# Kernel tuning notes

Hardware: AMD Instinct MI355X
Metric: run time of the kernel (lower is better)

## Reference

```python
import jax, jax.numpy as jnp
import numpy as np

N = 262144   # active voxels
C = 128      # channels (in == out)
B, Z, Y, X = 2, 41, 512, 512
EPS = 1e-3   # BN eps from norm_cfg


def _build_neighbors():
    """Build submanifold rulebook-style neighbor tables along z, y, x axes.
    Each table is [N, 3] (offsets -1, 0, +1); missing neighbor -> sentinel N
    (points at a zero-padded feature row)."""
    rng = np.random.default_rng(0)
    total = B * Z * Y * X
    lin = np.sort(rng.choice(total, size=N, replace=False)).astype(np.int64)
    lookup = np.full(total, -1, dtype=np.int64)
    lookup[lin] = np.arange(N)
    r = lin % (Z * Y * X)
    z = r // (Y * X)
    r2 = r % (Y * X)
    y = r2 // X
    x = r2 % X

    def nbrs(axis_vals, axis_size, stride):
        cols = []
        for off in (-1, 0, 1):
            v = axis_vals + off
            valid = (v >= 0) & (v < axis_size)
            nlin = np.clip(lin + off * stride, 0, total - 1)
            idx = np.where(valid, lookup[nlin], -1)
            idx = np.where(idx < 0, N, idx)
            cols.append(idx)
        return np.stack(cols, axis=1).astype(np.int32)

    return nbrs(z, Z, Y * X), nbrs(y, Y, X), nbrs(x, X, 1)


def setup_inputs() -> dict:
    key = jax.random.key(0)
    ks = jax.random.split(key, 8)
    nbr_z, nbr_y, nbr_x = _build_neighbors()
    scale = 1.0 / np.sqrt(3 * C)
    inp = {
        "features": jax.random.normal(ks[0], (N, C), dtype=jnp.float32),
        "W1": jax.random.normal(ks[1], (3, C, C), dtype=jnp.float32) * scale,  # conv3x1x1
        "W2": jax.random.normal(ks[2], (3, C, C), dtype=jnp.float32) * scale,  # conv1x3x1
        "W3": jax.random.normal(ks[3], (3, C, C), dtype=jnp.float32) * scale,  # conv1x1x3
        "g0": jax.random.normal(ks[4], (C,), dtype=jnp.float32) * 0.1 + 1.0,
        "b0": jnp.zeros((C,), dtype=jnp.float32),
        "m0": jax.random.normal(ks[5], (C,), dtype=jnp.float32) * 0.1,
        "v0": jax.random.uniform(ks[5], (C,), minval=0.5, maxval=1.5, dtype=jnp.float32),
        "g2": jax.random.normal(ks[6], (C,), dtype=jnp.float32) * 0.1 + 1.0,
        "b2": jnp.zeros((C,), dtype=jnp.float32),
        "m2": jax.random.normal(ks[6], (C,), dtype=jnp.float32) * 0.1,
        "v2": jax.random.uniform(ks[6], (C,), minval=0.5, maxval=1.5, dtype=jnp.float32),
        "g3": jax.random.normal(ks[7], (C,), dtype=jnp.float32) * 0.1 + 1.0,
        "b3": jnp.zeros((C,), dtype=jnp.float32),
        "m3": jax.random.normal(ks[7], (C,), dtype=jnp.float32) * 0.1,
        "v3": jax.random.uniform(ks[7], (C,), minval=0.5, maxval=1.5, dtype=jnp.float32),
        "nbr_z": jnp.asarray(nbr_z),
        "nbr_y": jnp.asarray(nbr_y),
        "nbr_x": jnp.asarray(nbr_x),
    }
    return inp


def _subm_conv(feats, nbr, W):
    # submanifold gather-matmul: out[n] = sum_k W[k] @ feats[nbr[n,k]] (sentinel -> 0)
    feats_pad = jnp.concatenate([feats, jnp.zeros((1, feats.shape[1]), feats.dtype)], axis=0)
    gathered = feats_pad[nbr]  # [N, 3, C]
    return jnp.einsum('nkc,kcd->nd', gathered, W)


def _bn(x, g, b, m, v):
    return (x - m) * (g * jax.lax.rsqrt(v + EPS)) + b


def reference(features, W1, W2, W3, g0, b0, m0, v0, g2, b2, m2, v2,
              g3, b3, m3, v3, nbr_z, nbr_y, nbr_x):
    # Branch 1: conv3x1x1 -> bn0 -> sigmoid, then (source bug) bn0_2 -> sigmoid applied again
    s = jax.nn.sigmoid(_bn(_subm_conv(features, nbr_z, W1), g0, b0, m0, v0))
    s = jax.nn.sigmoid(_bn(s, g2, b2, m2, v2))
    # Branch 2: conv1x3x1, added raw (its BN/act were mistakenly applied to branch 1)
    s2 = _subm_conv(features, nbr_y, W2)
    # Branch 3: conv1x1x3 -> bn0_3 -> sigmoid
    s3 = jax.nn.sigmoid(_bn(_subm_conv(features, nbr_x, W3), g3, b3, m3, v3))
    return (s + s2 + s3) * features
```

## Files before the change

### kernel.cpp

```cpp
#include <hip/hip_runtime.h>
#include <hip/hip_bf16.h>
#include <stdint.h>
#include <stddef.h>

#define NVOX 262144
#define CCH 128
#define BN_EPS 1e-3f

typedef __attribute__((ext_vector_type(8))) short bfrag;
typedef __attribute__((ext_vector_type(4))) float f4;

#define AS1 __attribute__((address_space(1)))
#define AS3 __attribute__((address_space(3)))

__device__ __forceinline__ unsigned short f2bf(float f) {
  union { float f; unsigned u; } v; v.f = f;
  unsigned r = v.u + 0x7fffu + ((v.u >> 16) & 1u);
  return (unsigned short)(r >> 16);
}

__device__ __forceinline__ bfrag pack8(f4 x, f4 y) {
  bfrag r;
  r[0] = (short)f2bf(x[0]); r[1] = (short)f2bf(x[1]);
  r[2] = (short)f2bf(x[2]); r[3] = (short)f2bf(x[3]);
  r[4] = (short)f2bf(y[0]); r[5] = (short)f2bf(y[1]);
  r[6] = (short)f2bf(y[2]); r[7] = (short)f2bf(y[3]);
  return r;
}

__device__ __forceinline__ float sigmoidf_(float x) {
  return 1.f / (1.f + __expf(-x));
}

__device__ __forceinline__ float bf2f(unsigned short h) {
  union { unsigned u; float f; } v; v.u = ((unsigned)h) << 16; return v.f;
}

__global__ void prep_wfrag(const float* __restrict__ W1, const float* __restrict__ W2,
                           const float* __restrict__ W3, unsigned short* __restrict__ wf) {
  const int frag = blockIdx.x;
  const int tile = frag & 7;
  const int kc   = (frag >> 3) & 3;
  const int tap  = (frag >> 5) % 3;
  const int conv = frag / 96;
  const float* W = (conv == 0) ? W1 : ((conv == 1) ? W2 : W3);
  const int l   = threadIdx.x;
  const int col = tile * 16 + (l & 15);
  const int k0  = kc * 32 + (l >> 4) * 8;
  bfrag o;
#pragma unroll
  for (int e = 0; e < 8; ++e)
    o[e] = (short)f2bf(W[(size_t)(tap * CCH + k0 + e) * CCH + col]);
  *reinterpret_cast<bfrag*>(wf + (size_t)frag * 512 + l * 8) = o;
}

__global__ void prep_bn(const float* g0, const float* b0, const float* m0, const float* v0,
                        const float* g2, const float* b2, const float* m2, const float* v2,
                        const float* g3, const float* b3, const float* m3, const float* v3,
                        float* __restrict__ bn) {
  const int c = threadIdx.x;
  const float s0 = g0[c] * rsqrtf(v0[c] + BN_EPS);
  const float s2 = g2[c] * rsqrtf(v2[c] + BN_EPS);
  const float s3 = g3[c] * rsqrtf(v3[c] + BN_EPS);
  bn[0 * CCH + c] = s0; bn[1 * CCH + c] = b0[c] - m0[c] * s0;
  bn[2 * CCH + c] = s2; bn[3 * CCH + c] = b2[c] - m2[c] * s2;
  bn[4 * CCH + c] = s3; bn[5 * CCH + c] = b3[c] - m3[c] * s3;
}

__global__ void prep_bf16(const float* __restrict__ feats, unsigned short* __restrict__ fbf) {
  const size_t base = ((size_t)blockIdx.x * 256 + threadIdx.x) * 8;
  const f4 x = *reinterpret_cast<const f4*>(feats + base);
  const f4 y = *reinterpret_cast<const f4*>(feats + base + 4);
  *reinterpret_cast<bfrag*>(fbf + base) = pack8(x, y);
  if (blockIdx.x == 0 && threadIdx.x < 16) {
    bfrag z = {0, 0, 0, 0, 0, 0, 0, 0};
    *reinterpret_cast<bfrag*>(fbf + (size_t)NVOX * CCH + threadIdx.x * 8) = z;
  }
}

__global__ __launch_bounds__(512, 4)
void recon_v11(const unsigned short* __restrict__ fbf,
               const unsigned short* __restrict__ wfrag,
               const float* __restrict__ bn,
               const int* __restrict__ nbrz, const int* __restrict__ nbrx,
               const int* __restrict__ nbry,
               float* __restrict__ out) {
  __shared__ unsigned short Bb[24576];

  const int tid  = threadIdx.x;
  const int lane = tid & 63;
  const int w    = tid >> 6;
  const int l15  = lane & 15;
  const int lhi  = lane >> 4;
  const int cb   = blockIdx.x & 1;
  const int row0 = (blockIdx.x >> 1) * 128;
  const int wrow = row0 + w * 16;

  auto fillconv = [&](int RB) {
#pragma unroll
    for (int i = 0; i < 6; ++i) {
      const int L    = w * 6 + i;
      const int slot = L >> 4;
      const int sub  = L & 15;
      const int g    = ((RB + slot) * 4 + (sub >> 2)) * 8 + cb * 4 + (sub & 3);
      __builtin_amdgcn_global_load_lds(
          (const AS1 void*)(wfrag + (size_t)g * 512 + lane * 8),
          (AS3 void*)((char*)Bb + L * 1024), 16, 0, 0);
    }
  };

  fillconv(0);
  const int row = wrow + l15;
  const int rg  = row * 3;
  const int izp = nbrz[rg + 0], izn = nbrz[rg + 2];
  const int ixp = nbrx[rg + 0], ixn = nbrx[rg + 2];
  const int iyp = nbry[rg + 0], iyn = nbry[rg + 2];

  const bool azp = __any(izp != NVOX), azn = __any(izn != NVOX);
  const bool axp = __any(ixp != NVOX), axn = __any(ixn != NVOX);
  const bool ayp = __any(iyp != NVOX), ayn = __any(iyn != NVOX);

  bfrag aF[4];
  bfrag aS[4];

#define LOADF(DST, IDX) {                                                     \
    const char* p = (const char*)fbf + ((size_t)(unsigned)(IDX) << 8) + (lhi << 4); \
    DST[0] = *reinterpret_cast<const bfrag*>(p);                              \
    DST[1] = *reinterpret_cast<const bfrag*>(p + 64);                         \
    DST[2] = *reinterpret_cast<const bfrag*>(p + 128);                        \
    DST[3] = *reinterpret_cast<const bfrag*>(p + 192);                        \
  }

#define TAP(SLOT, AFR, ACCS) {                                                \
    const char* bs = (const char*)Bb + (SLOT) * 16384 + lane * 16;            \
    _Pragma("unroll")                                                         \
    for (int kc = 0; kc < 4; ++kc) {                                          \
      _Pragma("unroll")                                                       \
      for (int ct = 0; ct < 4; ++ct) {                                        \
        const bfrag b = *reinterpret_cast<const bfrag*>(                      \
            bs + (kc * 4 + ct) * 1024);                                       \
        ACCS[ct] = __builtin_amdgcn_mfma_f32_16x16x32_bf16(                   \
            AFR[kc], b, ACCS[ct], 0, 0, 0);                                   \
      } } }

#define CONV(VP, VN, IP, IN, ACCS)                                            \
  {                                                                           \
    if (VP)      LOADF(aF, IP)                                                \
    else if (VN) LOADF(aF, IN)                                                \
    TAP(1, aS, ACCS)                                                          \
    if (VP) {                                                                 \
      TAP(0, aF, ACCS)                                                        \
      if (VN) { LOADF(aF, IN)  TAP(2, aF, ACCS) }                             \
    } else if (VN) {                                                          \
      TAP(2, aF, ACCS)                                                        \
    }                                                                         \
  }

  LOADF(aS, row)

  __syncthreads();

  f4 acc[4], run[4];
#pragma unroll
  for (int ct = 0; ct < 4; ++ct) {
    acc[ct] = f4{0.f, 0.f, 0.f, 0.f};
    run[ct] = f4{0.f, 0.f, 0.f, 0.f};
  }

  CONV(azp, azn, izp, izn, acc)
  __syncthreads();
  fillconv(6);
#pragma unroll
  for (int ct = 0; ct < 4; ++ct) {
    const int col = cb * 64 + ct * 16 + l15;
    const float sc0 = bn[0 * CCH + col], sh0 = bn[1 * CCH + col];
    const float sc2 = bn[2 * CCH + col], sh2 = bn[3 * CCH + col];
#pragma unroll
    for (int j = 0; j < 4; ++j) {
      const float u = sigmoidf_(sc0 * acc[ct][j] + sh0);
      run[ct][j] = sigmoidf_(sc2 * u + sh2);
    }
    acc[ct] = f4{0.f, 0.f, 0.f, 0.f};
  }
  __syncthreads();

  CONV(axp, axn, ixp, ixn, acc)
  __syncthreads();
  fillconv(3);
#pragma unroll
  for (int ct = 0; ct < 4; ++ct) {
    const int col = cb * 64 + ct * 16 + l15;
    const float sc3 = bn[4 * CCH + col], sh3 = bn[5 * CCH + col];
#pragma unroll
    for (int j = 0; j < 4; ++j)
      run[ct][j] += sigmoidf_(sc3 * acc[ct][j] + sh3);
  }
  __syncthreads();

  CONV(ayp, ayn, iyp, iyn, run)

#undef CONV
#undef TAP
#undef LOADF

#pragma unroll
  for (int ct = 0; ct < 4; ++ct) {
    const int col = cb * 64 + ct * 16 + l15;
#pragma unroll
    for (int j = 0; j < 4; ++j) {
      const int r = wrow + (lhi << 2) + j;
      const size_t o = ((size_t)r << 7) + col;
      out[o] = run[ct][j] * bf2f(fbf[o]);
    }
  }
}

__global__ void recon_naive(const float* __restrict__ feats,
    const float* __restrict__ W1, const float* __restrict__ W2, const float* __restrict__ W3,
    const int* __restrict__ nbrz, const int* __restrict__ nbry, const int* __restrict__ nbrx,
    const float* g0, const float* b0, const float* m0, const float* v0,
    const float* g2, const float* b2, const float* m2, const float* v2,
    const float* g3, const float* b3, const float* m3, const float* v3,
    float* __restrict__ out) {
  __shared__ float rows[3][CCH];
  const int n = blockIdx.x;
  const int d = threadIdx.x;
  float res[3];
#pragma unroll
  for (int conv = 0; conv < 3; ++conv) {
    const int* nbr  = (conv == 0) ? nbrz : ((conv == 1) ? nbry : nbrx);
    const float* W  = (conv == 0) ? W1 : ((conv == 1) ? W2 : W3);
#pragma unroll
    for (int tap = 0; tap < 3; ++tap) {
      const int idx = nbr[n * 3 + tap];
      rows[tap][d] = ((unsigned)idx < (unsigned)NVOX) ? feats[((size_t)idx << 7) + d] : 0.f;
    }
    __syncthreads();
    const float* rflat = &rows[0][0];
    float s = 0.f;
    for (int k = 0; k < 3 * CCH; ++k) s += rflat[k] * W[(size_t)k * CCH + d];
    res[conv] = s;
    __syncthreads();
  }
  const float sc0 = g0[d] * rsqrtf(v0[d] + BN_EPS), sh0 = b0[d] - m0[d] * sc0;
  const float sc2 = g2[d] * rsqrtf(v2[d] + BN_EPS), sh2 = b2[d] - m2[d] * sc2;
  const float sc3 = g3[d] * rsqrtf(v3[d] + BN_EPS), sh3 = b3[d] - m3[d] * sc3;
  float u = sigmoidf_(sc0 * res[0] + sh0);
  u = sigmoidf_(sc2 * u + sh2);
  const float s3v = sigmoidf_(sc3 * res[2] + sh3);
  out[((size_t)n << 7) + d] = (u + res[1] + s3v) * feats[((size_t)n << 7) + d];
}

extern "C" void kernel_launch(void* const* d_in, const int* in_sizes, int n_in,
                              void* d_out, int out_size, void* d_ws, size_t ws_size,
                              hipStream_t stream) {
  const float* feats = (const float*)d_in[0];
  const float* W1 = (const float*)d_in[1];
  const float* W2 = (const float*)d_in[2];
  const float* W3 = (const float*)d_in[3];
  const float* g0 = (const float*)d_in[4];
  const float* b0 = (const float*)d_in[5];
  const float* m0 = (const float*)d_in[6];
  const float* v0 = (const float*)d_in[7];
  const float* g2 = (const float*)d_in[8];
  const float* b2 = (const float*)d_in[9];
  const float* m2 = (const float*)d_in[10];
  const float* v2 = (const float*)d_in[11];
  const float* g3 = (const float*)d_in[12];
  const float* b3 = (const float*)d_in[13];
  const float* m3 = (const float*)d_in[14];
  const float* v3 = (const float*)d_in[15];
  const int* nz = (const int*)d_in[16];
  const int* ny = (const int*)d_in[17];
  const int* nx = (const int*)d_in[18];
  float* out = (float*)d_out;

  const size_t wf_bytes = 288u * 1024u;
  const size_t bn_bytes = 4096u;
  const size_t fb_bytes = ((size_t)NVOX + 1) * CCH * sizeof(short);
  if (ws_size >= wf_bytes + bn_bytes + fb_bytes) {
    unsigned short* wf  = (unsigned short*)d_ws;
    float*          bnt = (float*)((char*)d_ws + wf_bytes);
    unsigned short* fbf = (unsigned short*)((char*)d_ws + wf_bytes + bn_bytes);
    hipLaunchKernelGGL(prep_wfrag, dim3(288), dim3(64), 0, stream, W1, W2, W3, wf);
    hipLaunchKernelGGL(prep_bn, dim3(1), dim3(CCH), 0, stream,
                       g0, b0, m0, v0, g2, b2, m2, v2, g3, b3, m3, v3, bnt);
    hipLaunchKernelGGL(prep_bf16, dim3((NVOX * CCH) / (256 * 8)), dim3(256), 0, stream,
                       feats, fbf);
    hipLaunchKernelGGL(recon_v11, dim3((NVOX / 128) * 2), dim3(512), 0, stream,
                       fbf, wf, bnt, nz, nx, ny, out);
  } else {
    hipLaunchKernelGGL(recon_naive, dim3(NVOX), dim3(CCH), 0, stream,
                       feats, W1, W2, W3, nz, ny, nx,
                       g0, b0, m0, v0, g2, b2, m2, v2, g3, b3, m3, v3, out);
  }
}
```

Before: 149.8 us.

## Process two 16-row tiles per wave to reuse LDS weight fragments

Each wave now computes 32 rows instead of 16, issuing two MFMAs per weight fragment read from LDS. This halves LDS weight traffic and the weight fill per output row, and halves the grid size. A block-index swizzle spreads the 8 blocks of each group across distant row ranges. The centre-tap feature load is no longer kept in registers across convs: it is reloaded per conv, and the tap-skip branches are simplified. Register pressure doubles for the accumulators, which may hurt occupancy under launch_bounds(512,4).

```diff
diff --git a/kernel.cpp b/kernel.cpp
--- a/kernel.cpp
+++ b/kernel.cpp
@@ -79,7 +79,7 @@
 }
 
 __global__ __launch_bounds__(512, 4)
-void recon_v11(const unsigned short* __restrict__ fbf,
+void recon_v12(const unsigned short* __restrict__ fbf,
                const unsigned short* __restrict__ wfrag,
                const float* __restrict__ bn,
                const int* __restrict__ nbrz, const int* __restrict__ nbrx,
@@ -92,9 +92,10 @@
   const int w    = tid >> 6;
   const int l15  = lane & 15;
   const int lhi  = lane >> 4;
-  const int cb   = blockIdx.x & 1;
-  const int row0 = (blockIdx.x >> 1) * 128;
-  const int wrow = row0 + w * 16;
+  const int bid  = ((blockIdx.x & 7) << 8) + (blockIdx.x >> 3);
+  const int cb   = bid & 1;
+  const int row0 = (bid >> 1) << 8;
+  const int wrow = row0 + w * 32;
 
   auto fillconv = [&](int RB) {
 #pragma unroll
@@ -110,18 +111,24 @@
   };
 
   fillconv(0);
-  const int row = wrow + l15;
-  const int rg  = row * 3;
-  const int izp = nbrz[rg + 0], izn = nbrz[rg + 2];
-  const int ixp = nbrx[rg + 0], ixn = nbrx[rg + 2];
-  const int iyp = nbry[rg + 0], iyn = nbry[rg + 2];
-
-  const bool azp = __any(izp != NVOX), azn = __any(izn != NVOX);
-  const bool axp = __any(ixp != NVOX), axn = __any(ixn != NVOX);
-  const bool ayp = __any(iyp != NVOX), ayn = __any(iyn != NVOX);
-
-  bfrag aF[4];
-  bfrag aS[4];
+  const int rowA = wrow + l15;
+  const int rowB = rowA + 16;
+  const int rgA = rowA * 3, rgB = rowB * 3;
+  const int izpA = nbrz[rgA + 0], iznA = nbrz[rgA + 2];
+  const int izpB = nbrz[rgB + 0], iznB = nbrz[rgB + 2];
+  const int ixpA = nbrx[rgA + 0], ixnA = nbrx[rgA + 2];
+  const int ixpB = nbrx[rgB + 0], ixnB = nbrx[rgB + 2];
+  const int iypA = nbry[rgA + 0], iynA = nbry[rgA + 2];
+  const int iypB = nbry[rgB + 0], iynB = nbry[rgB + 2];
+
+  const bool azp = __any((izpA != NVOX) || (izpB != NVOX));
+  const bool azn = __any((iznA != NVOX) || (iznB != NVOX));
+  const bool axp = __any((ixpA != NVOX) || (ixpB != NVOX));
+  const bool axn = __any((ixnA != NVOX) || (ixnB != NVOX));
+  const bool ayp = __any((iypA != NVOX) || (iypB != NVOX));
+  const bool ayn = __any((iynA != NVOX) || (iynB != NVOX));
+
+  bfrag aX[4], aY[4];
 
 #define LOADF(DST, IDX) {                                                     \
     const char* p = (const char*)fbf + ((size_t)(unsigned)(IDX) << 8) + (lhi << 4); \
@@ -131,7 +138,7 @@
     DST[3] = *reinterpret_cast<const bfrag*>(p + 192);                        \
   }
 
-#define TAP(SLOT, AFR, ACCS) {                                                \
+#define TAP2(SLOT, A0, A1) {                                                  \
     const char* bs = (const char*)Bb + (SLOT) * 16384 + lane * 16;            \
     _Pragma("unroll")                                                         \
     for (int kc = 0; kc < 4; ++kc) {                                          \
@@ -139,35 +146,27 @@
       for (int ct = 0; ct < 4; ++ct) {                                        \
         const bfrag b = *reinterpret_cast<const bfrag*>(                      \
             bs + (kc * 4 + ct) * 1024);                                       \
-        ACCS[ct] = __builtin_amdgcn_mfma_f32_16x16x32_bf16(                   \
-            AFR[kc], b, ACCS[ct], 0, 0, 0);                                   \
+        A0[ct] = __builtin_amdgcn_mfma_f32_16x16x32_bf16(aX[kc], b, A0[ct], 0, 0, 0); \
+        A1[ct] = __builtin_amdgcn_mfma_f32_16x16x32_bf16(aY[kc], b, A1[ct], 0, 0, 0); \
       } } }
 
-#define CONV(VP, VN, IP, IN, ACCS)                                            \
+#define CONV(VP, VN, IPA, IPB, INA, INB, A0, A1)                              \
   {                                                                           \
-    if (VP)      LOADF(aF, IP)                                                \
-    else if (VN) LOADF(aF, IN)                                                \
-    TAP(1, aS, ACCS)                                                          \
-    if (VP) {                                                                 \
-      TAP(0, aF, ACCS)                                                        \
-      if (VN) { LOADF(aF, IN)  TAP(2, aF, ACCS) }                             \
-    } else if (VN) {                                                          \
-      TAP(2, aF, ACCS)                                                        \
-    }                                                                         \
-  }
-
-  LOADF(aS, row)
-
-  __syncthreads();
-
-  f4 acc[4], run[4];
+    if (VP) { LOADF(aX, IPA)  LOADF(aY, IPB)  TAP2(0, A0, A1) }               \
+    LOADF(aX, rowA)  LOADF(aY, rowB)  TAP2(1, A0, A1)                         \
+    if (VN) { LOADF(aX, INA)  LOADF(aY, INB)  TAP2(2, A0, A1) }               \
+  }
+
+  __syncthreads();
+
+  f4 acc0[4], acc1[4], run0[4], run1[4];
 #pragma unroll
   for (int ct = 0; ct < 4; ++ct) {
-    acc[ct] = f4{0.f, 0.f, 0.f, 0.f};
-    run[ct] = f4{0.f, 0.f, 0.f, 0.f};
-  }
-
-  CONV(azp, azn, izp, izn, acc)
+    acc0[ct] = f4{0.f, 0.f, 0.f, 0.f};
+    acc1[ct] = f4{0.f, 0.f, 0.f, 0.f};
+  }
+
+  CONV(azp, azn, izpA, izpB, iznA, iznB, acc0, acc1)
   __syncthreads();
   fillconv(6);
 #pragma unroll
@@ -177,14 +176,17 @@
     const float sc2 = bn[2 * CCH + col], sh2 = bn[3 * CCH + col];
 #pragma unroll
     for (int j = 0; j < 4; ++j) {
-      const float u = sigmoidf_(sc0 * acc[ct][j] + sh0);
-      run[ct][j] = sigmoidf_(sc2 * u + sh2);
-    }
-    acc[ct] = f4{0.f, 0.f, 0.f, 0.f};
-  }
-  __syncthreads();
-
-  CONV(axp, axn, ixp, ixn, acc)
+      const float u0 = sigmoidf_(sc0 * acc0[ct][j] + sh0);
+      run0[ct][j] = sigmoidf_(sc2 * u0 + sh2);
+      const float u1 = sigmoidf_(sc0 * acc1[ct][j] + sh0);
+      run1[ct][j] = sigmoidf_(sc2 * u1 + sh2);
+    }
+    acc0[ct] = f4{0.f, 0.f, 0.f, 0.f};
+    acc1[ct] = f4{0.f, 0.f, 0.f, 0.f};
+  }
+  __syncthreads();
+
+  CONV(axp, axn, ixpA, ixpB, ixnA, ixnB, acc0, acc1)
   __syncthreads();
   fillconv(3);
 #pragma unroll
@@ -192,15 +194,17 @@
     const int col = cb * 64 + ct * 16 + l15;
     const float sc3 = bn[4 * CCH + col], sh3 = bn[5 * CCH + col];
 #pragma unroll
-    for (int j = 0; j < 4; ++j)
-      run[ct][j] += sigmoidf_(sc3 * acc[ct][j] + sh3);
-  }
-  __syncthreads();
-
-  CONV(ayp, ayn, iyp, iyn, run)
+    for (int j = 0; j < 4; ++j) {
+      run0[ct][j] += sigmoidf_(sc3 * acc0[ct][j] + sh3);
+      run1[ct][j] += sigmoidf_(sc3 * acc1[ct][j] + sh3);
+    }
+  }
+  __syncthreads();
+
+  CONV(ayp, ayn, iypA, iypB, iynA, iynB, run0, run1)
 
 #undef CONV
-#undef TAP
+#undef TAP2
 #undef LOADF
 
 #pragma unroll
@@ -208,9 +212,12 @@
     const int col = cb * 64 + ct * 16 + l15;
 #pragma unroll
     for (int j = 0; j < 4; ++j) {
-      const int r = wrow + (lhi << 2) + j;
-      const size_t o = ((size_t)r << 7) + col;
-      out[o] = run[ct][j] * bf2f(fbf[o]);
+      const int r0 = wrow + (lhi << 2) + j;
+      const size_t o0 = ((size_t)r0 << 7) + col;
+      out[o0] = run0[ct][j] * bf2f(fbf[o0]);
+      const int r1 = r0 + 16;
+      const size_t o1 = ((size_t)r1 << 7) + col;
+      out[o1] = run1[ct][j] * bf2f(fbf[o1]);
     }
   }
 }
@@ -287,7 +294,7 @@
                        g0, b0, m0, v0, g2, b2, m2, v2, g3, b3, m3, v3, bnt);
     hipLaunchKernelGGL(prep_bf16, dim3((NVOX * CCH) / (256 * 8)), dim3(256), 0, stream,
                        feats, fbf);
-    hipLaunchKernelGGL(recon_v11, dim3((NVOX / 128) * 2), dim3(512), 0, stream,
+    hipLaunchKernelGGL(recon_v12, dim3((NVOX / 256) * 2), dim3(512), 0, stream,
                        fbf, wf, bnt, nz, nx, ny, out);
   } else {
     hipLaunchKernelGGL(recon_naive, dim3(NVOX), dim3(CCH), 0, stream,
```

Result: slower. 182.8 us (+22.0%).
